# Kernel optimization log

Hardware: AMD Instinct MI355X
Metric: run time of the kernel (lower is better)

The kernel has to match this reference:

```python
import jax, jax.numpy as jnp
import numpy as np

B, S, DM = 2, 2048, 1024
H, D = 16, 64  # num_heads, head_dim
EPS = 1e-5


def setup_inputs() -> dict:
    key = jax.random.key(0)
    ks = jax.random.split(key, 5)
    sc = 1.0 / np.sqrt(DM)
    return {
        "x": jax.random.normal(ks[0], (B, S, DM), jnp.float32),
        "wq": jax.random.normal(ks[1], (DM, DM), jnp.float32) * sc,
        "bq": jnp.zeros((DM,), jnp.float32),
        "wk": jax.random.normal(ks[2], (DM, DM), jnp.float32) * sc,
        "bk": jnp.zeros((DM,), jnp.float32),
        "wv": jax.random.normal(ks[3], (DM, DM), jnp.float32) * sc,
        "bv": jnp.zeros((DM,), jnp.float32),
        "wo": jax.random.normal(ks[4], (DM, DM), jnp.float32) * sc,
        "bo": jnp.zeros((DM,), jnp.float32),
        "alpha": jnp.ones((1,), jnp.float32),
    }


def reference(x, wq, bq, wk, bk, wv, bv, wo, bo, alpha):
    b, s, _ = x.shape
    # QKV projections -> [B, S, H, D]
    q = (x @ wq + bq).reshape(b, s, H, D)
    k = (x @ wk + bk).reshape(b, s, H, D)
    v = (x @ wv + bv).reshape(b, s, H, D)
    # YAT scores: (Q.K)^2 / (||Q-K||^2 + eps)
    dot = jnp.einsum("bqhd,bkhd->bhqk", q, k)  # [B,H,S,S]
    qn = jnp.einsum("bqhd,bqhd->bhq", q, q)    # ||q||^2
    kn = jnp.einsum("bkhd,bkhd->bhk", k, k)    # ||k||^2
    dist2 = qn[..., :, None] + kn[..., None, :] - 2.0 * dot
    scores = (dot * dot) / (dist2 + EPS)
    # alpha scaling: (sqrt(D)/log(1+D))^alpha
    scale = (jnp.sqrt(jnp.float32(D)) / jnp.log1p(jnp.float32(D))) ** alpha[0]
    attn = jax.nn.softmax(scores * scale, axis=-1)
    out = jnp.einsum("bhqk,bkhd->bqhd", attn, v).reshape(b, s, H * D)
    return out @ wo + bo
```

## Files before the change

kernel.cpp:

```cpp
#include <hip/hip_runtime.h>
#include <hip/hip_bf16.h>
#include <math.h>

typedef __bf16 bf16;
typedef bf16 bf16x4 __attribute__((ext_vector_type(4)));
typedef bf16 bf16x8 __attribute__((ext_vector_type(8)));
typedef float floatx4 __attribute__((ext_vector_type(4)));

#define MFMA16(a, b, c) __builtin_amdgcn_mfma_f32_16x16x32_bf16(a, b, c, 0, 0, 0)

__device__ __forceinline__ void split2(float v, bf16& h, bf16& l) {
    h = (bf16)v;
    l = (bf16)(v - (float)h);
}

__device__ __forceinline__ void gload16(const bf16* g, bf16* l) {
    __builtin_amdgcn_global_load_lds(
        (const __attribute__((address_space(1))) void*)g,
        (__attribute__((address_space(3))) void*)l, 16, 0, 0);
}

__global__ void prep_kernel(const float* __restrict__ xf,
                            const float* __restrict__ wq, const float* __restrict__ wk,
                            const float* __restrict__ wv, const float* __restrict__ wo,
                            bf16* __restrict__ xh, bf16* __restrict__ xl,
                            bf16* __restrict__ wt_qkv_h, bf16* __restrict__ wt_qkv_l,
                            bf16* __restrict__ wt_o_h) {
    const int z = blockIdx.z;
    if (z == 4) {
        const int tid = threadIdx.y * 32 + threadIdx.x;
        const int bid = blockIdx.y * 32 + blockIdx.x;
        const size_t i = ((size_t)bid * 256 + tid) * 16;
#pragma unroll
        for (int half = 0; half < 2; half++) {
            float4 a = *(const float4*)(xf + i + half * 8);
            float4 b = *(const float4*)(xf + i + half * 8 + 4);
            bf16x8 oh, ol;
            float f[8] = {a.x, a.y, a.z, a.w, b.x, b.y, b.z, b.w};
#pragma unroll
            for (int j = 0; j < 8; j++) { bf16 h, l; split2(f[j], h, l); oh[j] = h; ol[j] = l; }
            *(bf16x8*)(xh + i + half * 8) = oh;
            *(bf16x8*)(xl + i + half * 8) = ol;
        }
        return;
    }
    const float* src = (z == 0) ? wq : (z == 1) ? wk : (z == 2) ? wv : wo;
    bf16* dsth = (z < 3) ? (wt_qkv_h + (size_t)z * 1024 * 1024) : wt_o_h;
    bf16* dstl = (z < 3) ? (wt_qkv_l + (size_t)z * 1024 * 1024) : nullptr;
    __shared__ float tile[32][33];
    const int x0 = blockIdx.x * 32, y0 = blockIdx.y * 32;
    const int tx = threadIdx.x, ty = threadIdx.y;
    for (int i = 0; i < 32; i += 8)
        tile[ty + i][tx] = src[(size_t)(y0 + ty + i) * 1024 + x0 + tx];
    __syncthreads();
    for (int i = 0; i < 32; i += 8) {
        bf16 h, l;
        split2(tile[tx][ty + i], h, l);
        dsth[(size_t)(x0 + ty + i) * 1024 + y0 + tx] = h;
        if (dstl) dstl[(size_t)(x0 + ty + i) * 1024 + y0 + tx] = l;
    }
}

__global__ __launch_bounds__(256, 2) void gemm_qk3(
    const bf16* __restrict__ Ah, const bf16* __restrict__ Al,
    const bf16* __restrict__ Bth, const bf16* __restrict__ Btl,
    const float* __restrict__ bq, const float* __restrict__ bk,
    bf16* __restrict__ Qh, bf16* __restrict__ Ql,
    bf16* __restrict__ Kh, bf16* __restrict__ Kl) {
    __shared__ bf16 Ash[128 * 32];
    __shared__ bf16 Asl[128 * 32];
    __shared__ bf16 Bsh[128 * 32];
    __shared__ bf16 Bsl[128 * 32];

    const int t = threadIdx.x;
    const int lane = t & 63, wave = t >> 6;
    const int quad = lane >> 4, l16 = lane & 15;
    const int m0 = blockIdx.x * 128, n0 = blockIdx.y * 128;
    const int wm = (wave >> 1) * 64, wn = (wave & 1) * 64;

    const int srow = wave * 16 + (lane >> 2);
    const int scol = (lane & 3) * 8;
    const bf16* gAh = Ah + (size_t)(m0 + srow) * 1024 + scol;
    const bf16* gAl = Al + (size_t)(m0 + srow) * 1024 + scol;
    const bf16* gBh = Bth + (size_t)(n0 + srow) * 1024 + scol;
    const bf16* gBl = Btl + (size_t)(n0 + srow) * 1024 + scol;
    bf16* lAh = &Ash[wave * 16 * 32];
    bf16* lAl = &Asl[wave * 16 * 32];
    bf16* lBh = &Bsh[wave * 16 * 32];
    bf16* lBl = &Bsl[wave * 16 * 32];

    floatx4 acc[4][4] = {};

    for (int k0 = 0; k0 < 1024; k0 += 32) {
        gload16(gAh + k0, lAh);
        gload16(gAh + 64 * 1024 + k0, lAh + 64 * 32);
        gload16(gBh + k0, lBh);
        gload16(gBh + 64 * 1024 + k0, lBh + 64 * 32);
        gload16(gAl + k0, lAl);
        gload16(gAl + 64 * 1024 + k0, lAl + 64 * 32);
        gload16(gBl + k0, lBl);
        gload16(gBl + 64 * 1024 + k0, lBl + 64 * 32);
        __syncthreads();
        bf16x8 afh[4], bfh[4], afl[4], bfl[4];
#pragma unroll
        for (int i = 0; i < 4; i++) {
            afh[i] = *(bf16x8*)&Ash[(wm + i * 16 + l16) * 32 + quad * 8];
            afl[i] = *(bf16x8*)&Asl[(wm + i * 16 + l16) * 32 + quad * 8];
        }
#pragma unroll
        for (int j = 0; j < 4; j++) {
            bfh[j] = *(bf16x8*)&Bsh[(wn + j * 16 + l16) * 32 + quad * 8];
            bfl[j] = *(bf16x8*)&Bsl[(wn + j * 16 + l16) * 32 + quad * 8];
        }
#pragma unroll
        for (int i = 0; i < 4; i++)
#pragma unroll
            for (int j = 0; j < 4; j++) {
                acc[i][j] = MFMA16(afh[i], bfh[j], acc[i][j]);
                acc[i][j] = MFMA16(afh[i], bfl[j], acc[i][j]);
                acc[i][j] = MFMA16(afl[i], bfh[j], acc[i][j]);
            }
        __syncthreads();
    }

    const int which = n0 >> 10;
    const float* bias = (which == 0) ? bq : bk;
    bf16* Dh = (which == 0) ? Qh : Kh;
    bf16* Dl = (which == 0) ? Ql : Kl;
#pragma unroll
    for (int i = 0; i < 4; i++)
#pragma unroll
        for (int j = 0; j < 4; j++) {
            const int col = n0 + wn + j * 16 + l16;
            const int o = col & 1023;
            const int h = o >> 6, d = o & 63;
            const float bvv = bias[o];
            const int gm0 = m0 + wm + i * 16 + quad * 4;
            const int b = gm0 >> 11;
#pragma unroll
            for (int r = 0; r < 4; r++) {
                const int gm = gm0 + r;
                const int s = gm & 2047;
                const size_t idx = (size_t)((b * 16 + h) * 2048 + s) * 64 + d;
                const float val = acc[i][j][r] + bvv;
                bf16 hi, lo;
                split2(val, hi, lo);
                Dh[idx] = hi;
                Dl[idx] = lo;
            }
        }
}

__global__ __launch_bounds__(256, 2) void gemm_v(
    const bf16* __restrict__ Ah, const bf16* __restrict__ Bth,
    const float* __restrict__ bv, bf16* __restrict__ VtG) {
    __shared__ bf16 As[128 * 32];
    __shared__ bf16 Bs[128 * 32];

    const int t = threadIdx.x;
    const int lane = t & 63, wave = t >> 6;
    const int quad = lane >> 4, l16 = lane & 15;
    const int m0 = blockIdx.x * 128, n0 = blockIdx.y * 128;
    const int wm = (wave >> 1) * 64, wn = (wave & 1) * 64;

    const int srow = wave * 16 + (lane >> 2);
    const int scol = (lane & 3) * 8;
    const bf16* gA0 = Ah + (size_t)(m0 + srow) * 1024 + scol;
    const bf16* gB0 = Bth + (size_t)(2048 + n0 + srow) * 1024 + scol;
    bf16* lA = &As[wave * 16 * 32];
    bf16* lB = &Bs[wave * 16 * 32];

    floatx4 acc[4][4] = {};

    for (int k0 = 0; k0 < 1024; k0 += 32) {
        gload16(gA0 + k0, lA);
        gload16(gA0 + 64 * 1024 + k0, lA + 64 * 32);
        gload16(gB0 + k0, lB);
        gload16(gB0 + 64 * 1024 + k0, lB + 64 * 32);
        __syncthreads();
        bf16x8 af[4], bf_[4];
#pragma unroll
        for (int i = 0; i < 4; i++)
            af[i] = *(bf16x8*)&As[(wm + i * 16 + l16) * 32 + quad * 8];
#pragma unroll
        for (int j = 0; j < 4; j++)
            bf_[j] = *(bf16x8*)&Bs[(wn + j * 16 + l16) * 32 + quad * 8];
#pragma unroll
        for (int i = 0; i < 4; i++)
#pragma unroll
            for (int j = 0; j < 4; j++)
                acc[i][j] = MFMA16(af[i], bf_[j], acc[i][j]);
        __syncthreads();
    }

#pragma unroll
    for (int i = 0; i < 4; i++)
#pragma unroll
        for (int j = 0; j < 4; j++) {
            const int o = (n0 + wn + j * 16 + l16) & 1023;
            const int h = o >> 6, d = o & 63;
            const float bvv = bv[o];
            const int gm0 = m0 + wm + i * 16 + quad * 4;
            const int b = gm0 >> 11;
            bf16x4 pv;
#pragma unroll
            for (int r = 0; r < 4; r++) pv[r] = (bf16)(acc[i][j][r] + bvv);
            const int s0 = gm0 & 2047;
            *(bf16x4*)&VtG[((size_t)((b * 16 + h) * 64 + d)) * 2048 + s0] = pv;
        }
}

__global__ void kn_kernel(const bf16* __restrict__ Kh, const bf16* __restrict__ Kl,
                          float* __restrict__ knG) {
    const int i = blockIdx.x * 256 + threadIdx.x;
    const bf16* ph = Kh + (size_t)i * 64;
    const bf16* pl = Kl + (size_t)i * 64;
    float s = 0.f;
#pragma unroll
    for (int d0 = 0; d0 < 64; d0 += 8) {
        bf16x8 vh = *(const bf16x8*)(ph + d0);
        bf16x8 vl = *(const bf16x8*)(pl + d0);
#pragma unroll
        for (int j = 0; j < 8; j++) { float x = (float)vh[j] + (float)vl[j]; s += x * x; }
    }
    knG[i] = s;
}

__global__ __launch_bounds__(256, 2) void attn_kernel(
    const bf16* __restrict__ Qh, const bf16* __restrict__ Ql,
    const bf16* __restrict__ Kh, const bf16* __restrict__ Kl,
    const bf16* __restrict__ VtG, const float* __restrict__ knG,
    bf16* __restrict__ O, const float* __restrict__ alphap) {
    __shared__ bf16 Ksh[2][64 * 72];
    __shared__ bf16 Ksl[2][64 * 72];
    __shared__ bf16 Vs[2][64 * 72];
    __shared__ bf16 Pt[4][32 * 72];
    __shared__ float knL[2][64];

    const int t = threadIdx.x, lane = t & 63, wave = t >> 6;
    const int quad = lane >> 4, l16 = lane & 15;
    const int bh = blockIdx.x;
    const int qw = blockIdx.y * 128 + wave * 32;

    const float alpha = alphap[0];
    const float C = powf(8.0f / log1pf(64.0f), alpha) * 1.44269504f;

    const size_t qrow0 = ((size_t)bh * 2048 + qw + l16) * 64;
    const size_t qrow1 = qrow0 + 16 * 64;
    bf16x8 bq0h[2], bq1h[2], bq0l[2], bq1l[2];
    bq0h[0] = *(const bf16x8*)(Qh + qrow0 + quad * 8);
    bq1h[0] = *(const bf16x8*)(Qh + qrow0 + 32 + quad * 8);
    bq0l[0] = *(const bf16x8*)(Ql + qrow0 + quad * 8);
    bq1l[0] = *(const bf16x8*)(Ql + qrow0 + 32 + quad * 8);
    bq0h[1] = *(const bf16x8*)(Qh + qrow1 + quad * 8);
    bq1h[1] = *(const bf16x8*)(Qh + qrow1 + 32 + quad * 8);
    bq0l[1] = *(const bf16x8*)(Ql + qrow1 + quad * 8);
    bq1l[1] = *(const bf16x8*)(Ql + qrow1 + 32 + quad * 8);

    float qne[2];
#pragma unroll
    for (int qg = 0; qg < 2; qg++) {
        float qn = 0.f;
#pragma unroll
        for (int j = 0; j < 8; j++) {
            float x0 = (float)bq0h[qg][j] + (float)bq0l[qg][j];
            float x1 = (float)bq1h[qg][j] + (float)bq1l[qg][j];
            qn += x0 * x0 + x1 * x1;
        }
        qn += __shfl_xor(qn, 16, 64);
        qn += __shfl_xor(qn, 32, 64);
        qne[qg] = qn + 1e-5f;
    }

    floatx4 acco[2][4] = {};
    float l_i[2] = {0.f, 0.f};

    const int srow = t >> 3;
    const int scol = (t & 7) * 8;
    const size_t vrow0 = ((size_t)bh * 64 + srow) * 2048;
    const size_t vrow1 = ((size_t)bh * 64 + srow + 32) * 2048;
    const float* knB = knG + (size_t)bh * 2048;

    auto do_chunk = [&](int ib) {
        const bf16* KshC = Ksh[ib];
        const bf16* KslC = Ksl[ib];
        const bf16* VsC = Vs[ib];
        const float* knC = knL[ib];
        bf16* Pw = Pt[wave];
        float rs0 = 0.f, rs1 = 0.f;
#pragma unroll
        for (int sub = 0; sub < 4; sub++) {
            bf16x8 a0h = *(bf16x8*)&KshC[(sub * 16 + l16) * 72 + quad * 8];
            bf16x8 a1h = *(bf16x8*)&KshC[(sub * 16 + l16) * 72 + 32 + quad * 8];
            bf16x8 a0l = *(bf16x8*)&KslC[(sub * 16 + l16) * 72 + quad * 8];
            bf16x8 a1l = *(bf16x8*)&KslC[(sub * 16 + l16) * 72 + 32 + quad * 8];
            floatx4 ac0 = {}, ac1 = {};
            ac0 = MFMA16(a0h, bq0h[0], ac0);
            ac0 = MFMA16(a1h, bq1h[0], ac0);
            ac0 = MFMA16(a0h, bq0l[0], ac0);
            ac0 = MFMA16(a1h, bq1l[0], ac0);
            ac0 = MFMA16(a0l, bq0h[0], ac0);
            ac0 = MFMA16(a1l, bq1h[0], ac0);
            ac1 = MFMA16(a0h, bq0h[1], ac1);
            ac1 = MFMA16(a1h, bq1h[1], ac1);
            ac1 = MFMA16(a0h, bq0l[1], ac1);
            ac1 = MFMA16(a1h, bq1l[1], ac1);
            ac1 = MFMA16(a0l, bq0h[1], ac1);
            ac1 = MFMA16(a1l, bq1h[1], ac1);
            const floatx4 knv = *(const floatx4*)&knC[sub * 16 + quad * 4];
            bf16x4 pv0, pv1;
#pragma unroll
            for (int r = 0; r < 4; r++) {
                const float d0 = ac0[r];
                const float d1 = ac1[r];
                const float e0 = fmaf(-2.0f, d0, qne[0] + knv[r]);
                const float e1 = fmaf(-2.0f, d1, qne[1] + knv[r]);
                const float t0 = C * d0 * d0;
                const float t1 = C * d1 * d1;
                const float s0 = fmaf(t0, __builtin_amdgcn_rcpf(e0), -110.0f);
                const float s1 = fmaf(t1, __builtin_amdgcn_rcpf(e1), -110.0f);
                const float p0 = __builtin_amdgcn_exp2f(s0);
                const float p1 = __builtin_amdgcn_exp2f(s1);
                rs0 += p0;
                rs1 += p1;
                pv0[r] = (bf16)p0;
                pv1[r] = (bf16)p1;
            }
            *(bf16x4*)&Pw[l16 * 72 + sub * 16 + quad * 4] = pv0;
            *(bf16x4*)&Pw[(16 + l16) * 72 + sub * 16 + quad * 4] = pv1;
        }
        rs0 += __shfl_xor(rs0, 16, 64);
        rs0 += __shfl_xor(rs0, 32, 64);
        rs1 += __shfl_xor(rs1, 16, 64);
        rs1 += __shfl_xor(rs1, 32, 64);
        l_i[0] += rs0;
        l_i[1] += rs1;

        bf16x8 bp0[2], bp1[2];
#pragma unroll
        for (int qg = 0; qg < 2; qg++) {
            bp0[qg] = *(bf16x8*)&Pw[(qg * 16 + l16) * 72 + quad * 8];
            bp1[qg] = *(bf16x8*)&Pw[(qg * 16 + l16) * 72 + 32 + quad * 8];
        }
#pragma unroll
        for (int dsub = 0; dsub < 4; dsub++) {
            bf16x8 a0 = *(bf16x8*)&VsC[(dsub * 16 + l16) * 72 + quad * 8];
            bf16x8 a1 = *(bf16x8*)&VsC[(dsub * 16 + l16) * 72 + 32 + quad * 8];
            acco[0][dsub] = MFMA16(a0, bp0[0], acco[0][dsub]);
            acco[0][dsub] = MFMA16(a1, bp1[0], acco[0][dsub]);
            acco[1][dsub] = MFMA16(a0, bp0[1], acco[1][dsub]);
            acco[1][dsub] = MFMA16(a1, bp1[1], acco[1][dsub]);
        }
    };

    {
        const size_t kb = (size_t)(bh * 2048) * 64;
        bf16x8 k0 = *(const bf16x8*)(Kh + kb + srow * 64 + scol);
        bf16x8 k1 = *(const bf16x8*)(Kh + kb + (32 + srow) * 64 + scol);
        bf16x8 c0 = *(const bf16x8*)(Kl + kb + srow * 64 + scol);
        bf16x8 c1 = *(const bf16x8*)(Kl + kb + (32 + srow) * 64 + scol);
        bf16x8 v0 = *(const bf16x8*)(VtG + vrow0 + scol);
        bf16x8 v1 = *(const bf16x8*)(VtG + vrow1 + scol);
        *(bf16x8*)&Ksh[0][srow * 72 + scol] = k0;
        *(bf16x8*)&Ksh[0][(32 + srow) * 72 + scol] = k1;
        *(bf16x8*)&Ksl[0][srow * 72 + scol] = c0;
        *(bf16x8*)&Ksl[0][(32 + srow) * 72 + scol] = c1;
        *(bf16x8*)&Vs[0][srow * 72 + scol] = v0;
        *(bf16x8*)&Vs[0][(32 + srow) * 72 + scol] = v1;
        if (t < 16) *(float4*)&knL[0][t * 4] = *(const float4*)(knB + t * 4);
    }
    __syncthreads();

    for (int ic = 0; ic < 31; ic++) {
        const int cur = ic & 1, nxt = cur ^ 1;
        const int kc = (ic + 1) * 64;
        const size_t kb = (size_t)(bh * 2048 + kc) * 64;
        bf16x8 nk0 = *(const bf16x8*)(Kh + kb + srow * 64 + scol);
        bf16x8 nk1 = *(const bf16x8*)(Kh + kb + (32 + srow) * 64 + scol);
        bf16x8 nc0 = *(const bf16x8*)(Kl + kb + srow * 64 + scol);
        bf16x8 nc1 = *(const bf16x8*)(Kl + kb + (32 + srow) * 64 + scol);
        bf16x8 nv0 = *(const bf16x8*)(VtG + vrow0 + kc + scol);
        bf16x8 nv1 = *(const bf16x8*)(VtG + vrow1 + kc + scol);
        float4 nkn;
        if (t < 16) nkn = *(const float4*)(knB + kc + t * 4);

        do_chunk(cur);

        *(bf16x8*)&Ksh[nxt][srow * 72 + scol] = nk0;
        *(bf16x8*)&Ksh[nxt][(32 + srow) * 72 + scol] = nk1;
        *(bf16x8*)&Ksl[nxt][srow * 72 + scol] = nc0;
        *(bf16x8*)&Ksl[nxt][(32 + srow) * 72 + scol] = nc1;
        *(bf16x8*)&Vs[nxt][srow * 72 + scol] = nv0;
        *(bf16x8*)&Vs[nxt][(32 + srow) * 72 + scol] = nv1;
        if (t < 16) *(float4*)&knL[nxt][t * 4] = nkn;
        __syncthreads();
    }
    do_chunk(1);

    const int b = bh >> 4, h = bh & 15;
#pragma unroll
    for (int qg = 0; qg < 2; qg++) {
        const int s = qw + qg * 16 + l16;
        const float rl = 1.0f / l_i[qg];
        const size_t obase = (size_t)(b * 2048 + s) * 1024 + h * 64;
#pragma unroll
        for (int dsub = 0; dsub < 4; dsub++) {
            bf16x4 ov;
#pragma unroll
            for (int r = 0; r < 4; r++) ov[r] = (bf16)(acco[qg][dsub][r] * rl);
            *(bf16x4*)&O[obase + dsub * 16 + quad * 4] = ov;
        }
    }
}

__global__ __launch_bounds__(256, 2) void gemm_out(
    const bf16* __restrict__ A, const bf16* __restrict__ Bt,
    const float* __restrict__ bias, float* __restrict__ outC) {
    __shared__ bf16 As[128 * 32];
    __shared__ bf16 Bs[128 * 32];

    const int t = threadIdx.x;
    const int lane = t & 63, wave = t >> 6;
    const int quad = lane >> 4, l16 = lane & 15;
    const int m0 = blockIdx.x * 128, n0 = blockIdx.y * 128;
    const int wm = (wave >> 1) * 64, wn = (wave & 1) * 64;

    const int srow = wave * 16 + (lane >> 2);
    const int scol = (lane & 3) * 8;
    const bf16* gA0 = A + (size_t)(m0 + srow) * 1024 + scol;
    const bf16* gB0 = Bt + (size_t)(n0 + srow) * 1024 + scol;
    bf16* lA = &As[wave * 16 * 32];
    bf16* lB = &Bs[wave * 16 * 32];

    floatx4 acc[4][4] = {};

    for (int k0 = 0; k0 < 1024; k0 += 32) {
        gload16(gA0 + k0, lA);
        gload16(gA0 + 64 * 1024 + k0, lA + 64 * 32);
        gload16(gB0 + k0, lB);
        gload16(gB0 + 64 * 1024 + k0, lB + 64 * 32);
        __syncthreads();
        bf16x8 af[4], bf_[4];
#pragma unroll
        for (int i = 0; i < 4; i++)
            af[i] = *(bf16x8*)&As[(wm + i * 16 + l16) * 32 + quad * 8];
#pragma unroll
        for (int j = 0; j < 4; j++)
            bf_[j] = *(bf16x8*)&Bs[(wn + j * 16 + l16) * 32 + quad * 8];
#pragma unroll
        for (int i = 0; i < 4; i++)
#pragma unroll
            for (int j = 0; j < 4; j++)
                acc[i][j] = MFMA16(af[i], bf_[j], acc[i][j]);
        __syncthreads();
    }

#pragma unroll
    for (int i = 0; i < 4; i++)
#pragma unroll
        for (int j = 0; j < 4; j++) {
            const int col = n0 + wn + j * 16 + l16;
            const float bvv = bias[col];
#pragma unroll
            for (int r = 0; r < 4; r++) {
                const int gm = m0 + wm + i * 16 + quad * 4 + r;
                outC[(size_t)gm * 1024 + col] = acc[i][j][r] + bvv;
            }
        }
}

extern "C" void kernel_launch(void* const* d_in, const int* in_sizes, int n_in,
                              void* d_out, int out_size, void* d_ws, size_t ws_size,
                              hipStream_t stream) {
    const float* x  = (const float*)d_in[0];
    const float* wq = (const float*)d_in[1];
    const float* bq = (const float*)d_in[2];
    const float* wk = (const float*)d_in[3];
    const float* bk = (const float*)d_in[4];
    const float* wv = (const float*)d_in[5];
    const float* bv = (const float*)d_in[6];
    const float* wo = (const float*)d_in[7];
    const float* bo = (const float*)d_in[8];
    const float* alpha = (const float*)d_in[9];

    char* ws = (char*)d_ws;
    const size_t MB = 1024 * 1024;
    bf16* wqkv_h = (bf16*)(ws);
    bf16* wqkv_l = (bf16*)(ws + 6 * MB);
    bf16* wo_h   = (bf16*)(ws + 12 * MB);
    float* knG   = (float*)(ws + 14 * MB);
    bf16* x_h    = (bf16*)(ws + 16 * MB);
    bf16* x_l    = (bf16*)(ws + 24 * MB);
    bf16* Q_h    = (bf16*)(ws + 32 * MB);
    bf16* Q_l    = (bf16*)(ws + 40 * MB);
    bf16* K_h    = (bf16*)(ws + 48 * MB);
    bf16* K_l    = (bf16*)(ws + 56 * MB);
    bf16* Vt_g   = (bf16*)(ws + 64 * MB);
    bf16* Ob     = (bf16*)(ws);

    prep_kernel<<<dim3(32, 32, 5), dim3(32, 8), 0, stream>>>(
        x, wq, wk, wv, wo, x_h, x_l, wqkv_h, wqkv_l, wo_h);
    gemm_qk3<<<dim3(32, 16), 256, 0, stream>>>(
        x_h, x_l, wqkv_h, wqkv_l, bq, bk, Q_h, Q_l, K_h, K_l);
    gemm_v<<<dim3(32, 8), 256, 0, stream>>>(x_h, wqkv_h, bv, Vt_g);
    kn_kernel<<<dim3(256), 256, 0, stream>>>(K_h, K_l, knG);
    attn_kernel<<<dim3(32, 16), 256, 0, stream>>>(
        Q_h, Q_l, K_h, K_l, Vt_g, knG, Ob, alpha);
    gemm_out<<<dim3(32, 8), 256, 0, stream>>>(Ob, wo_h, bo, (float*)d_out);
}
```

Before: 282.9 us.

## Use 32x32 MFMA in attention with register-resident P and swizzled LDS

The attention kernel moves from 16x16x32 to 32x32x16 bf16 MFMA tiles. The probability matrix is now packed with v_cvt_pk_bf16_f32 and rearranged across lanes with v_permlane32_swap, so it stays in registers instead of round-tripping through a shared-memory Pt buffer. K/V shared tiles drop the padded stride in favour of an XOR swizzle to avoid bank conflicts. Separately, the V-projection and output GEMMs switch to 128x64 tiles, doubling the grid to improve occupancy at the cost of less operand reuse per block.

```diff
diff --git a/kernel.cpp b/kernel.cpp
--- a/kernel.cpp
+++ b/kernel.cpp
@@ -6,12 +6,24 @@
 typedef bf16 bf16x4 __attribute__((ext_vector_type(4)));
 typedef bf16 bf16x8 __attribute__((ext_vector_type(8)));
 typedef float floatx4 __attribute__((ext_vector_type(4)));
+typedef float floatx16 __attribute__((ext_vector_type(16)));
 
 #define MFMA16(a, b, c) __builtin_amdgcn_mfma_f32_16x16x32_bf16(a, b, c, 0, 0, 0)
+#define MFMA32(a, b, c) __builtin_amdgcn_mfma_f32_32x32x16_bf16(a, b, c, 0, 0, 0)
 
 __device__ __forceinline__ void split2(float v, bf16& h, bf16& l) {
     h = (bf16)v;
     l = (bf16)(v - (float)h);
+}
+
+__device__ __forceinline__ unsigned cvt_pk(float lo, float hi) {
+    unsigned r;
+    asm("v_cvt_pk_bf16_f32 %0, %1, %2" : "=v"(r) : "v"(lo), "v"(hi));
+    return r;
+}
+
+__device__ __forceinline__ void pl32swap(unsigned& a, unsigned& b) {
+    asm("v_permlane32_swap_b32 %0, %1" : "+v"(a), "+v"(b));
 }
 
 __device__ __forceinline__ void gload16(const bf16* g, bf16* l) {
@@ -155,13 +167,13 @@
     const bf16* __restrict__ Ah, const bf16* __restrict__ Bth,
     const float* __restrict__ bv, bf16* __restrict__ VtG) {
     __shared__ bf16 As[128 * 32];
-    __shared__ bf16 Bs[128 * 32];
+    __shared__ bf16 Bs[64 * 32];
 
     const int t = threadIdx.x;
     const int lane = t & 63, wave = t >> 6;
     const int quad = lane >> 4, l16 = lane & 15;
-    const int m0 = blockIdx.x * 128, n0 = blockIdx.y * 128;
-    const int wm = (wave >> 1) * 64, wn = (wave & 1) * 64;
+    const int m0 = blockIdx.x * 128, n0 = blockIdx.y * 64;
+    const int wm = (wave >> 1) * 64, wn = (wave & 1) * 32;
 
     const int srow = wave * 16 + (lane >> 2);
     const int scol = (lane & 3) * 8;
@@ -170,25 +182,24 @@
     bf16* lA = &As[wave * 16 * 32];
     bf16* lB = &Bs[wave * 16 * 32];
 
-    floatx4 acc[4][4] = {};
+    floatx4 acc[4][2] = {};
 
     for (int k0 = 0; k0 < 1024; k0 += 32) {
         gload16(gA0 + k0, lA);
         gload16(gA0 + 64 * 1024 + k0, lA + 64 * 32);
         gload16(gB0 + k0, lB);
-        gload16(gB0 + 64 * 1024 + k0, lB + 64 * 32);
-        __syncthreads();
-        bf16x8 af[4], bf_[4];
+        __syncthreads();
+        bf16x8 af[4], bf_[2];
 #pragma unroll
         for (int i = 0; i < 4; i++)
             af[i] = *(bf16x8*)&As[(wm + i * 16 + l16) * 32 + quad * 8];
 #pragma unroll
-        for (int j = 0; j < 4; j++)
+        for (int j = 0; j < 2; j++)
             bf_[j] = *(bf16x8*)&Bs[(wn + j * 16 + l16) * 32 + quad * 8];
 #pragma unroll
         for (int i = 0; i < 4; i++)
 #pragma unroll
-            for (int j = 0; j < 4; j++)
+            for (int j = 0; j < 2; j++)
                 acc[i][j] = MFMA16(af[i], bf_[j], acc[i][j]);
         __syncthreads();
     }
@@ -196,7 +207,7 @@
 #pragma unroll
     for (int i = 0; i < 4; i++)
 #pragma unroll
-        for (int j = 0; j < 4; j++) {
+        for (int j = 0; j < 2; j++) {
             const int o = (n0 + wn + j * 16 + l16) & 1023;
             const int h = o >> 6, d = o & 63;
             const float bvv = bv[o];
@@ -231,142 +242,138 @@
     const bf16* __restrict__ Kh, const bf16* __restrict__ Kl,
     const bf16* __restrict__ VtG, const float* __restrict__ knG,
     bf16* __restrict__ O, const float* __restrict__ alphap) {
-    __shared__ bf16 Ksh[2][64 * 72];
-    __shared__ bf16 Ksl[2][64 * 72];
-    __shared__ bf16 Vs[2][64 * 72];
-    __shared__ bf16 Pt[4][32 * 72];
-    __shared__ float knL[2][64];
+    __shared__ bf16 Ksh[2][64 * 64];
+    __shared__ bf16 Ksl[2][64 * 64];
+    __shared__ bf16 Vs[2][64 * 64];
+    __shared__ __align__(16) float knL[2][64];
 
     const int t = threadIdx.x, lane = t & 63, wave = t >> 6;
-    const int quad = lane >> 4, l16 = lane & 15;
+    const int l31 = lane & 31, h = lane >> 5;
     const int bh = blockIdx.x;
     const int qw = blockIdx.y * 128 + wave * 32;
 
     const float alpha = alphap[0];
     const float C = powf(8.0f / log1pf(64.0f), alpha) * 1.44269504f;
 
-    const size_t qrow0 = ((size_t)bh * 2048 + qw + l16) * 64;
-    const size_t qrow1 = qrow0 + 16 * 64;
-    bf16x8 bq0h[2], bq1h[2], bq0l[2], bq1l[2];
-    bq0h[0] = *(const bf16x8*)(Qh + qrow0 + quad * 8);
-    bq1h[0] = *(const bf16x8*)(Qh + qrow0 + 32 + quad * 8);
-    bq0l[0] = *(const bf16x8*)(Ql + qrow0 + quad * 8);
-    bq1l[0] = *(const bf16x8*)(Ql + qrow0 + 32 + quad * 8);
-    bq0h[1] = *(const bf16x8*)(Qh + qrow1 + quad * 8);
-    bq1h[1] = *(const bf16x8*)(Qh + qrow1 + 32 + quad * 8);
-    bq0l[1] = *(const bf16x8*)(Ql + qrow1 + quad * 8);
-    bq1l[1] = *(const bf16x8*)(Ql + qrow1 + 32 + quad * 8);
-
-    float qne[2];
-#pragma unroll
-    for (int qg = 0; qg < 2; qg++) {
-        float qn = 0.f;
+    const size_t qbase = ((size_t)bh * 2048 + qw + l31) * 64;
+    bf16x8 bqh[4], bql[4];
+#pragma unroll
+    for (int cb = 0; cb < 4; cb++) {
+        bqh[cb] = *(const bf16x8*)(Qh + qbase + cb * 16 + h * 8);
+        bql[cb] = *(const bf16x8*)(Ql + qbase + cb * 16 + h * 8);
+    }
+    float qn = 0.f;
+#pragma unroll
+    for (int cb = 0; cb < 4; cb++)
 #pragma unroll
         for (int j = 0; j < 8; j++) {
-            float x0 = (float)bq0h[qg][j] + (float)bq0l[qg][j];
-            float x1 = (float)bq1h[qg][j] + (float)bq1l[qg][j];
-            qn += x0 * x0 + x1 * x1;
-        }
-        qn += __shfl_xor(qn, 16, 64);
-        qn += __shfl_xor(qn, 32, 64);
-        qne[qg] = qn + 1e-5f;
-    }
-
-    floatx4 acco[2][4] = {};
-    float l_i[2] = {0.f, 0.f};
+            float x = (float)bqh[cb][j] + (float)bql[cb][j];
+            qn += x * x;
+        }
+    qn += __shfl_xor(qn, 32, 64);
+    const float qne = qn + 1e-5f;
+
+    floatx16 acco[2] = {};
+    float l_run = 0.f;
 
     const int srow = t >> 3;
     const int scol = (t & 7) * 8;
+    const int smask = (srow & 7) * 8;
+    const int so0 = srow * 64 + (scol ^ smask);
+    const int so1 = (srow + 32) * 64 + (scol ^ smask);
     const size_t vrow0 = ((size_t)bh * 64 + srow) * 2048;
-    const size_t vrow1 = ((size_t)bh * 64 + srow + 32) * 2048;
+    const size_t vrow1 = vrow0 + (size_t)32 * 2048;
     const float* knB = knG + (size_t)bh * 2048;
 
+    const int fmask = (l31 & 7) * 8;
+    int foff[2][4];
+#pragma unroll
+    for (int rb = 0; rb < 2; rb++)
+#pragma unroll
+        for (int cb = 0; cb < 4; cb++)
+            foff[rb][cb] = (rb * 32 + l31) * 64 + ((cb * 16 + h * 8) ^ fmask);
+
     auto do_chunk = [&](int ib) {
-        const bf16* KshC = Ksh[ib];
-        const bf16* KslC = Ksl[ib];
-        const bf16* VsC = Vs[ib];
+        const bf16* KH = Ksh[ib];
+        const bf16* KL = Ksl[ib];
+        const bf16* VV = Vs[ib];
         const float* knC = knL[ib];
-        bf16* Pw = Pt[wave];
-        float rs0 = 0.f, rs1 = 0.f;
-#pragma unroll
-        for (int sub = 0; sub < 4; sub++) {
-            bf16x8 a0h = *(bf16x8*)&KshC[(sub * 16 + l16) * 72 + quad * 8];
-            bf16x8 a1h = *(bf16x8*)&KshC[(sub * 16 + l16) * 72 + 32 + quad * 8];
-            bf16x8 a0l = *(bf16x8*)&KslC[(sub * 16 + l16) * 72 + quad * 8];
-            bf16x8 a1l = *(bf16x8*)&KslC[(sub * 16 + l16) * 72 + 32 + quad * 8];
-            floatx4 ac0 = {}, ac1 = {};
-            ac0 = MFMA16(a0h, bq0h[0], ac0);
-            ac0 = MFMA16(a1h, bq1h[0], ac0);
-            ac0 = MFMA16(a0h, bq0l[0], ac0);
-            ac0 = MFMA16(a1h, bq1l[0], ac0);
-            ac0 = MFMA16(a0l, bq0h[0], ac0);
-            ac0 = MFMA16(a1l, bq1h[0], ac0);
-            ac1 = MFMA16(a0h, bq0h[1], ac1);
-            ac1 = MFMA16(a1h, bq1h[1], ac1);
-            ac1 = MFMA16(a0h, bq0l[1], ac1);
-            ac1 = MFMA16(a1h, bq1l[1], ac1);
-            ac1 = MFMA16(a0l, bq0h[1], ac1);
-            ac1 = MFMA16(a1l, bq1h[1], ac1);
-            const floatx4 knv = *(const floatx4*)&knC[sub * 16 + quad * 4];
-            bf16x4 pv0, pv1;
-#pragma unroll
-            for (int r = 0; r < 4; r++) {
-                const float d0 = ac0[r];
-                const float d1 = ac1[r];
-                const float e0 = fmaf(-2.0f, d0, qne[0] + knv[r]);
-                const float e1 = fmaf(-2.0f, d1, qne[1] + knv[r]);
-                const float t0 = C * d0 * d0;
-                const float t1 = C * d1 * d1;
-                const float s0 = fmaf(t0, __builtin_amdgcn_rcpf(e0), -110.0f);
-                const float s1 = fmaf(t1, __builtin_amdgcn_rcpf(e1), -110.0f);
-                const float p0 = __builtin_amdgcn_exp2f(s0);
-                const float p1 = __builtin_amdgcn_exp2f(s1);
-                rs0 += p0;
-                rs1 += p1;
-                pv0[r] = (bf16)p0;
-                pv1[r] = (bf16)p1;
-            }
-            *(bf16x4*)&Pw[l16 * 72 + sub * 16 + quad * 4] = pv0;
-            *(bf16x4*)&Pw[(16 + l16) * 72 + sub * 16 + quad * 4] = pv1;
-        }
-        rs0 += __shfl_xor(rs0, 16, 64);
-        rs0 += __shfl_xor(rs0, 32, 64);
-        rs1 += __shfl_xor(rs1, 16, 64);
-        rs1 += __shfl_xor(rs1, 32, 64);
-        l_i[0] += rs0;
-        l_i[1] += rs1;
-
-        bf16x8 bp0[2], bp1[2];
-#pragma unroll
-        for (int qg = 0; qg < 2; qg++) {
-            bp0[qg] = *(bf16x8*)&Pw[(qg * 16 + l16) * 72 + quad * 8];
-            bp1[qg] = *(bf16x8*)&Pw[(qg * 16 + l16) * 72 + 32 + quad * 8];
-        }
-#pragma unroll
-        for (int dsub = 0; dsub < 4; dsub++) {
-            bf16x8 a0 = *(bf16x8*)&VsC[(dsub * 16 + l16) * 72 + quad * 8];
-            bf16x8 a1 = *(bf16x8*)&VsC[(dsub * 16 + l16) * 72 + 32 + quad * 8];
-            acco[0][dsub] = MFMA16(a0, bp0[0], acco[0][dsub]);
-            acco[0][dsub] = MFMA16(a1, bp1[0], acco[0][dsub]);
-            acco[1][dsub] = MFMA16(a0, bp0[1], acco[1][dsub]);
-            acco[1][dsub] = MFMA16(a1, bp1[1], acco[1][dsub]);
-        }
+
+        floatx16 acc[2] = {};
+#pragma unroll
+        for (int cb = 0; cb < 4; cb++)
+#pragma unroll
+            for (int kb = 0; kb < 2; kb++) {
+                bf16x8 ah = *(const bf16x8*)&KH[foff[kb][cb]];
+                bf16x8 al = *(const bf16x8*)&KL[foff[kb][cb]];
+                acc[kb] = MFMA32(ah, bqh[cb], acc[kb]);
+                acc[kb] = MFMA32(ah, bql[cb], acc[kb]);
+                acc[kb] = MFMA32(al, bqh[cb], acc[kb]);
+            }
+
+        unsigned pw[2][8];
+        float rs = 0.f;
+#pragma unroll
+        for (int kb = 0; kb < 2; kb++) {
+            float p[16];
+#pragma unroll
+            for (int g2 = 0; g2 < 4; g2++) {
+                const floatx4 knv = *(const floatx4*)&knC[kb * 32 + g2 * 8 + h * 4];
+#pragma unroll
+                for (int j = 0; j < 4; j++) {
+                    const int r = g2 * 4 + j;
+                    const float d = acc[kb][r];
+                    const float e = fmaf(-2.0f, d, qne + knv[j]);
+                    const float s = fmaf(C * d * d, __builtin_amdgcn_rcpf(e), -110.0f);
+                    const float pp = __builtin_amdgcn_exp2f(s);
+                    rs += pp;
+                    p[r] = pp;
+                }
+            }
+#pragma unroll
+            for (int g = 0; g < 2; g++) {
+                unsigned a0 = cvt_pk(p[8 * g + 0], p[8 * g + 1]);
+                unsigned a1 = cvt_pk(p[8 * g + 2], p[8 * g + 3]);
+                unsigned b0 = cvt_pk(p[8 * g + 4], p[8 * g + 5]);
+                unsigned b1 = cvt_pk(p[8 * g + 6], p[8 * g + 7]);
+                pl32swap(a0, b0);
+                pl32swap(a1, b1);
+                pw[kb][g * 4 + 0] = a0;
+                pw[kb][g * 4 + 1] = a1;
+                pw[kb][g * 4 + 2] = b0;
+                pw[kb][g * 4 + 3] = b1;
+            }
+        }
+        l_run += rs;
+
+#pragma unroll
+        for (int db = 0; db < 2; db++)
+#pragma unroll
+            for (int g4 = 0; g4 < 4; g4++) {
+                bf16x8 vf = *(const bf16x8*)&VV[foff[db][g4]];
+                union { unsigned u[4]; bf16x8 v; } pu;
+                pu.u[0] = pw[g4 >> 1][(g4 & 1) * 4 + 0];
+                pu.u[1] = pw[g4 >> 1][(g4 & 1) * 4 + 1];
+                pu.u[2] = pw[g4 >> 1][(g4 & 1) * 4 + 2];
+                pu.u[3] = pw[g4 >> 1][(g4 & 1) * 4 + 3];
+                acco[db] = MFMA32(vf, pu.v, acco[db]);
+            }
     };
 
     {
-        const size_t kb = (size_t)(bh * 2048) * 64;
-        bf16x8 k0 = *(const bf16x8*)(Kh + kb + srow * 64 + scol);
-        bf16x8 k1 = *(const bf16x8*)(Kh + kb + (32 + srow) * 64 + scol);
-        bf16x8 c0 = *(const bf16x8*)(Kl + kb + srow * 64 + scol);
-        bf16x8 c1 = *(const bf16x8*)(Kl + kb + (32 + srow) * 64 + scol);
+        const size_t kb0 = (size_t)(bh * 2048) * 64;
+        bf16x8 k0 = *(const bf16x8*)(Kh + kb0 + srow * 64 + scol);
+        bf16x8 k1 = *(const bf16x8*)(Kh + kb0 + (32 + srow) * 64 + scol);
+        bf16x8 c0 = *(const bf16x8*)(Kl + kb0 + srow * 64 + scol);
+        bf16x8 c1 = *(const bf16x8*)(Kl + kb0 + (32 + srow) * 64 + scol);
         bf16x8 v0 = *(const bf16x8*)(VtG + vrow0 + scol);
         bf16x8 v1 = *(const bf16x8*)(VtG + vrow1 + scol);
-        *(bf16x8*)&Ksh[0][srow * 72 + scol] = k0;
-        *(bf16x8*)&Ksh[0][(32 + srow) * 72 + scol] = k1;
-        *(bf16x8*)&Ksl[0][srow * 72 + scol] = c0;
-        *(bf16x8*)&Ksl[0][(32 + srow) * 72 + scol] = c1;
-        *(bf16x8*)&Vs[0][srow * 72 + scol] = v0;
-        *(bf16x8*)&Vs[0][(32 + srow) * 72 + scol] = v1;
+        *(bf16x8*)&Ksh[0][so0] = k0;
+        *(bf16x8*)&Ksh[0][so1] = k1;
+        *(bf16x8*)&Ksl[0][so0] = c0;
+        *(bf16x8*)&Ksl[0][so1] = c1;
+        *(bf16x8*)&Vs[0][so0] = v0;
+        *(bf16x8*)&Vs[0][so1] = v1;
         if (t < 16) *(float4*)&knL[0][t * 4] = *(const float4*)(knB + t * 4);
     }
     __syncthreads();
@@ -374,11 +381,11 @@
     for (int ic = 0; ic < 31; ic++) {
         const int cur = ic & 1, nxt = cur ^ 1;
         const int kc = (ic + 1) * 64;
-        const size_t kb = (size_t)(bh * 2048 + kc) * 64;
-        bf16x8 nk0 = *(const bf16x8*)(Kh + kb + srow * 64 + scol);
-        bf16x8 nk1 = *(const bf16x8*)(Kh + kb + (32 + srow) * 64 + scol);
-        bf16x8 nc0 = *(const bf16x8*)(Kl + kb + srow * 64 + scol);
-        bf16x8 nc1 = *(const bf16x8*)(Kl + kb + (32 + srow) * 64 + scol);
+        const size_t kbg = (size_t)(bh * 2048 + kc) * 64;
+        bf16x8 nk0 = *(const bf16x8*)(Kh + kbg + srow * 64 + scol);
+        bf16x8 nk1 = *(const bf16x8*)(Kh + kbg + (32 + srow) * 64 + scol);
+        bf16x8 nc0 = *(const bf16x8*)(Kl + kbg + srow * 64 + scol);
+        bf16x8 nc1 = *(const bf16x8*)(Kl + kbg + (32 + srow) * 64 + scol);
         bf16x8 nv0 = *(const bf16x8*)(VtG + vrow0 + kc + scol);
         bf16x8 nv1 = *(const bf16x8*)(VtG + vrow1 + kc + scol);
         float4 nkn;
@@ -386,44 +393,45 @@
 
         do_chunk(cur);
 
-        *(bf16x8*)&Ksh[nxt][srow * 72 + scol] = nk0;
-        *(bf16x8*)&Ksh[nxt][(32 + srow) * 72 + scol] = nk1;
-        *(bf16x8*)&Ksl[nxt][srow * 72 + scol] = nc0;
-        *(bf16x8*)&Ksl[nxt][(32 + srow) * 72 + scol] = nc1;
-        *(bf16x8*)&Vs[nxt][srow * 72 + scol] = nv0;
-        *(bf16x8*)&Vs[nxt][(32 + srow) * 72 + scol] = nv1;
+        *(bf16x8*)&Ksh[nxt][so0] = nk0;
+        *(bf16x8*)&Ksh[nxt][so1] = nk1;
+        *(bf16x8*)&Ksl[nxt][so0] = nc0;
+        *(bf16x8*)&Ksl[nxt][so1] = nc1;
+        *(bf16x8*)&Vs[nxt][so0] = nv0;
+        *(bf16x8*)&Vs[nxt][so1] = nv1;
         if (t < 16) *(float4*)&knL[nxt][t * 4] = nkn;
         __syncthreads();
     }
     do_chunk(1);
 
-    const int b = bh >> 4, h = bh & 15;
-#pragma unroll
-    for (int qg = 0; qg < 2; qg++) {
-        const int s = qw + qg * 16 + l16;
-        const float rl = 1.0f / l_i[qg];
-        const size_t obase = (size_t)(b * 2048 + s) * 1024 + h * 64;
-#pragma unroll
-        for (int dsub = 0; dsub < 4; dsub++) {
+    const float l_tot = l_run + __shfl_xor(l_run, 32, 64);
+    const float rl = 1.0f / l_tot;
+    const int b = bh >> 4, hh = bh & 15;
+    const int q = qw + l31;
+    const size_t obase = (size_t)(b * 2048 + q) * 1024 + hh * 64;
+#pragma unroll
+    for (int db = 0; db < 2; db++)
+#pragma unroll
+        for (int g2 = 0; g2 < 4; g2++) {
             bf16x4 ov;
 #pragma unroll
-            for (int r = 0; r < 4; r++) ov[r] = (bf16)(acco[qg][dsub][r] * rl);
-            *(bf16x4*)&O[obase + dsub * 16 + quad * 4] = ov;
-        }
-    }
+            for (int j = 0; j < 4; j++) ov[j] = (bf16)(acco[db][g2 * 4 + j] * rl);
+            const int d = db * 32 + g2 * 8 + h * 4;
+            *(bf16x4*)&O[obase + d] = ov;
+        }
 }
 
 __global__ __launch_bounds__(256, 2) void gemm_out(
     const bf16* __restrict__ A, const bf16* __restrict__ Bt,
     const float* __restrict__ bias, float* __restrict__ outC) {
     __shared__ bf16 As[128 * 32];
-    __shared__ bf16 Bs[128 * 32];
+    __shared__ bf16 Bs[64 * 32];
 
     const int t = threadIdx.x;
     const int lane = t & 63, wave = t >> 6;
     const int quad = lane >> 4, l16 = lane & 15;
-    const int m0 = blockIdx.x * 128, n0 = blockIdx.y * 128;
-    const int wm = (wave >> 1) * 64, wn = (wave & 1) * 64;
+    const int m0 = blockIdx.x * 128, n0 = blockIdx.y * 64;
+    const int wm = (wave >> 1) * 64, wn = (wave & 1) * 32;
 
     const int srow = wave * 16 + (lane >> 2);
     const int scol = (lane & 3) * 8;
@@ -432,25 +440,24 @@
     bf16* lA = &As[wave * 16 * 32];
     bf16* lB = &Bs[wave * 16 * 32];
 
-    floatx4 acc[4][4] = {};
+    floatx4 acc[4][2] = {};
 
     for (int k0 = 0; k0 < 1024; k0 += 32) {
         gload16(gA0 + k0, lA);
         gload16(gA0 + 64 * 1024 + k0, lA + 64 * 32);
         gload16(gB0 + k0, lB);
-        gload16(gB0 + 64 * 1024 + k0, lB + 64 * 32);
-        __syncthreads();
-        bf16x8 af[4], bf_[4];
+        __syncthreads();
+        bf16x8 af[4], bf_[2];
 #pragma unroll
         for (int i = 0; i < 4; i++)
             af[i] = *(bf16x8*)&As[(wm + i * 16 + l16) * 32 + quad * 8];
 #pragma unroll
-        for (int j = 0; j < 4; j++)
+        for (int j = 0; j < 2; j++)
             bf_[j] = *(bf16x8*)&Bs[(wn + j * 16 + l16) * 32 + quad * 8];
 #pragma unroll
         for (int i = 0; i < 4; i++)
 #pragma unroll
-            for (int j = 0; j < 4; j++)
+            for (int j = 0; j < 2; j++)
                 acc[i][j] = MFMA16(af[i], bf_[j], acc[i][j]);
         __syncthreads();
     }
@@ -458,7 +465,7 @@
 #pragma unroll
     for (int i = 0; i < 4; i++)
 #pragma unroll
-        for (int j = 0; j < 4; j++) {
+        for (int j = 0; j < 2; j++) {
             const int col = n0 + wn + j * 16 + l16;
             const float bvv = bias[col];
 #pragma unroll
@@ -502,9 +509,9 @@
         x, wq, wk, wv, wo, x_h, x_l, wqkv_h, wqkv_l, wo_h);
     gemm_qk3<<<dim3(32, 16), 256, 0, stream>>>(
         x_h, x_l, wqkv_h, wqkv_l, bq, bk, Q_h, Q_l, K_h, K_l);
-    gemm_v<<<dim3(32, 8), 256, 0, stream>>>(x_h, wqkv_h, bv, Vt_g);
+    gemm_v<<<dim3(32, 16), 256, 0, stream>>>(x_h, wqkv_h, bv, Vt_g);
     kn_kernel<<<dim3(256), 256, 0, stream>>>(K_h, K_l, knG);
     attn_kernel<<<dim3(32, 16), 256, 0, stream>>>(
         Q_h, Q_l, K_h, K_l, Vt_g, knG, Ob, alpha);
-    gemm_out<<<dim3(32, 8), 256, 0, stream>>>(Ob, wo_h, bo, (float*)d_out);
-}
+    gemm_out<<<dim3(32, 16), 256, 0, stream>>>(Ob, wo_h, bo, (float*)d_out);
+}
```

Measured after the change: 275.7 us. -2.5%, faster.
